# Optimization experiments

Measured on AMD Instinct MI355X. Metric: run time of the kernel, lower is better.

Reference implementation:

```python
import jax, jax.numpy as jnp
import numpy as np

B, N, E = 256, 10000, 160000
H1, H2 = 1024, 128


def setup_inputs() -> dict:
    key = jax.random.key(0)
    ks = jax.random.split(key, 8)
    data = jax.random.normal(ks[0], (B, N), dtype=jnp.float32)
    edge_index = jax.random.randint(ks[1], (2, E), 0, N, dtype=jnp.int64)
    # GCNConv(1, 1): scalar weight + scalar bias (Glorot-ish init)
    gcn_w = jax.random.normal(ks[2], (1,), dtype=jnp.float32)
    gcn_b = jnp.zeros((1,), dtype=jnp.float32)
    # encoder: Linear(N, 1024) -> ReLU -> Linear(1024, 128) -> ReLU
    W1 = jax.random.normal(ks[3], (N, H1), dtype=jnp.float32) * (1.0 / np.sqrt(N))
    b1 = jnp.zeros((H1,), dtype=jnp.float32)
    W2 = jax.random.normal(ks[4], (H1, H2), dtype=jnp.float32) * (1.0 / np.sqrt(H1))
    b2 = jnp.zeros((H2,), dtype=jnp.float32)
    return {"data": data, "gcn_w": gcn_w, "gcn_b": gcn_b,
            "W1": W1, "b1": b1, "W2": W2, "b2": b2,
            "edge_index": edge_index}


def reference(data, gcn_w, gcn_b, W1, b1, W2, b2, edge_index):
    n = data.shape[1]
    # PyG GCNConv defaults: add self-loops, symmetric normalization.
    loop = jnp.arange(n, dtype=edge_index.dtype)
    src = jnp.concatenate([edge_index[0], loop])  # [E+N]
    dst = jnp.concatenate([edge_index[1], loop])
    deg = jax.ops.segment_sum(jnp.ones_like(dst, dtype=data.dtype), dst,
                              num_segments=n)  # >= 1 thanks to self-loops
    dinv = jax.lax.rsqrt(deg)
    norm = dinv[src] * dinv[dst]  # [E+N]
    # linear on 1-dim node features == scalar multiply, batched over B samples
    xw = data * gcn_w[0]                      # [B, N]
    msgs = xw[:, src] * norm                  # [B, E+N]
    agg = jax.ops.segment_sum(msgs.T, dst, num_segments=n).T  # [B, N]
    g = jax.nn.relu(agg + gcn_b[0])           # relu'd GCN output, one row per sample
    # dense MLP encoder (p_drop = 0 so dropout is identity)
    h = jax.nn.relu(g @ W1 + b1)              # [B, 1024]
    return jax.nn.relu(h @ W2 + b2)           # [B, 128]
```

## Files before the change

kernel.cpp:

```cpp
#include <hip/hip_runtime.h>
#include <hip/hip_bf16.h>


#define KPAD 10240
#define NSTEPS 10
#define ZSPLIT 16
#define ELLW 64

typedef __attribute__((ext_vector_type(8))) short short8v;
typedef __attribute__((ext_vector_type(4))) float f32x4;

__device__ inline short f2bf(float f) {
    union { float f; unsigned u; } v; v.f = f;
    unsigned r = v.u + 0x7fffu + ((v.u >> 16) & 1u);
    return (short)(r >> 16);
}

__device__ inline float bf2f(short s) {
    union { unsigned u; float f; } v;
    v.u = ((unsigned)(unsigned short)s) << 16;
    return v.f;
}

__device__ inline void gll16(const short* g, short* l) {
    __builtin_amdgcn_global_load_lds(
        (const __attribute__((address_space(1))) void*)g,
        (__attribute__((address_space(3))) void*)l, 16, 0, 0);
}

__global__ void pack_kernel(const float* __restrict__ data, const float* __restrict__ gw,
                            short* __restrict__ xwT, const float* __restrict__ W1,
                            short* __restrict__ W1T, float4* __restrict__ cntz,
                            int N, int B, int H1, int tTiles, int cTiles) {
    __shared__ short tile[32][66];
    int id = blockIdx.x, t = threadIdx.x;
    if (id < tTiles) {
        int nt = (N + 31) >> 5;
        int xb = id % nt, yb = id / nt;
        int n0 = xb * 32, b0 = yb * 32;
        float w = gw[0];
        int tx = t & 31, ty = t >> 5;
#pragma unroll
        for (int i = 0; i < 4; ++i) {
            int b = b0 + ty + i * 8;
            int n = n0 + tx;
            float v = (n < N) ? data[(size_t)b * N + n] : 0.f;
            tile[ty + i * 8][tx] = f2bf(v * w);
        }
        __syncthreads();
#pragma unroll
        for (int i = 0; i < 4; ++i) {
            int n = n0 + ty + i * 8;
            if (n < N) xwT[(size_t)n * B + b0 + tx] = tile[tx][ty + i * 8];
        }
    } else if (id < tTiles + cTiles) {
        int c = id - tTiles;
        int nk = KPAD >> 6;
        int kx = c % nk, hy = c / nk;
        int k0 = kx * 64, h0 = hy * 32;
        int hl = t & 31, kr = t >> 5;
#pragma unroll
        for (int i = 0; i < 8; ++i) {
            int k = k0 + kr + i * 8;
            float v = (k < N) ? W1[(size_t)k * H1 + h0 + hl] : 0.f;
            tile[hl][kr + i * 8] = f2bf(v);
        }
        __syncthreads();
        int kl = t & 63, hr = t >> 6;
#pragma unroll
        for (int i = 0; i < 8; ++i) {
            int h = h0 + hr + i * 4;
            W1T[(size_t)h * KPAD + k0 + kl] = tile[hr + i * 4][kl];
        }
    } else {
        int i = (id - tTiles - cTiles) * 256 + t;
        cntz[i] = make_float4(0.f, 0.f, 0.f, 0.f);
    }
}

__global__ void ell_fill(const int* __restrict__ ei, int* __restrict__ cnt,
                         int* __restrict__ ell, int E) {
    int e = blockIdx.x * blockDim.x + threadIdx.x;
    if (e >= E) return;
    int s = ei[e], d = ei[E + e];
    int c = atomicAdd(&cnt[d], 1);
    if (c < ELLW) ell[(d << 6) + c] = s;
}

__global__ void gather_kernel(const int* __restrict__ cnt, const int* __restrict__ ell,
                              const float* __restrict__ gcn_b, const short* __restrict__ xwT,
                              short* __restrict__ A0, int N, int B) {
    int row = blockIdx.x * 4 + (threadIdx.x >> 6);
    if (row >= N) return;
    int lane = threadIdx.x & 63;
    const short4* x4 = (const short4*)xwT;
    const int B4 = B >> 2;
    float gb = gcn_b[0];
    int dcnt = cnt[row];
    float di = rsqrtf((float)dcnt + 1.0f);
    float w = di * di;
    short4 v = x4[(size_t)row * B4 + lane];
    float ax = bf2f(v.x) * w, ay = bf2f(v.y) * w, az = bf2f(v.z) * w, aw = bf2f(v.w) * w;
    const int* er = ell + ((size_t)row << 6);
    int m = dcnt < ELLW ? dcnt : ELLW;
    int i = 0;
    for (; i + 1 < m; i += 2) {
        int s0 = er[i], s1 = er[i + 1];
        float n0 = rsqrtf((float)cnt[s0] + 1.0f) * di;
        float n1 = rsqrtf((float)cnt[s1] + 1.0f) * di;
        short4 u0 = x4[(size_t)s0 * B4 + lane];
        short4 u1 = x4[(size_t)s1 * B4 + lane];
        ax = fmaf(bf2f(u0.x), n0, ax); ay = fmaf(bf2f(u0.y), n0, ay);
        az = fmaf(bf2f(u0.z), n0, az); aw = fmaf(bf2f(u0.w), n0, aw);
        ax = fmaf(bf2f(u1.x), n1, ax); ay = fmaf(bf2f(u1.y), n1, ay);
        az = fmaf(bf2f(u1.z), n1, az); aw = fmaf(bf2f(u1.w), n1, aw);
    }
    if (i < m) {
        int s0 = er[i];
        float n0 = rsqrtf((float)cnt[s0] + 1.0f) * di;
        short4 u0 = x4[(size_t)s0 * B4 + lane];
        ax = fmaf(bf2f(u0.x), n0, ax); ay = fmaf(bf2f(u0.y), n0, ay);
        az = fmaf(bf2f(u0.z), n0, az); aw = fmaf(bf2f(u0.w), n0, aw);
    }
    short4 s4;
    s4.x = f2bf(fmaxf(ax + gb, 0.f));
    s4.y = f2bf(fmaxf(ay + gb, 0.f));
    s4.z = f2bf(fmaxf(az + gb, 0.f));
    s4.w = f2bf(fmaxf(aw + gb, 0.f));
    ((short4*)(A0 + (size_t)row * B))[lane] = s4;
}

__global__ void convertA(const short* __restrict__ A0, short* __restrict__ A, int K, int M) {
    __shared__ short tile[32][34];
    int k0 = blockIdx.x * 32, m0 = blockIdx.y * 32;
    int tx = threadIdx.x, ty = threadIdx.y;
#pragma unroll
    for (int i = 0; i < 4; ++i) {
        int k = k0 + ty + i * 8;
        short v = (k < K) ? A0[(size_t)k * M + m0 + tx] : (short)0;
        tile[tx][ty + i * 8] = v;
    }
    __syncthreads();
#pragma unroll
    for (int i = 0; i < 4; ++i) {
        int m = m0 + ty + i * 8;
        A[(size_t)m * KPAD + k0 + tx] = tile[ty + i * 8][tx];
    }
}

__global__ void __launch_bounds__(512)
gemm1_mfma(const short* __restrict__ A, const short* __restrict__ Wt,
           float* __restrict__ hpart) {
    __shared__ __align__(16) short ldsA[2][8192];
    __shared__ __align__(16) short ldsB[2][8192];
    const int n0 = blockIdx.x * 128;
    const int m0 = blockIdx.y * 128;
    const int kz = blockIdx.z * (NSTEPS * 64);
    const int t = threadIdx.x;
    const int l = t & 63, w = t >> 6;
    const int wm = w >> 2, wn = w & 3;
    const int q = l >> 4, i16 = l & 15;

    const int sRow = t & 127, sKq = t >> 7;
    const short* gA = A + (size_t)(m0 + sRow) * KPAD + kz + sKq * 8;
    const short* gB = Wt + (size_t)(n0 + sRow) * KPAD + kz + sKq * 8;
    const int ld0 = w * 512;
    const int ld1 = 4096 + w * 512;

    f32x4 acc[4][2];
#pragma unroll
    for (int mi = 0; mi < 4; ++mi)
#pragma unroll
        for (int ni = 0; ni < 2; ++ni) acc[mi][ni] = (f32x4){0.f, 0.f, 0.f, 0.f};

    gll16(gA, &ldsA[0][ld0]); gll16(gA + 32, &ldsA[0][ld1]);
    gll16(gB, &ldsB[0][ld0]); gll16(gB + 32, &ldsB[0][ld1]);
    gA += 64; gB += 64;

    for (int ks = 0; ks < NSTEPS; ++ks) {
        const int cur = ks & 1;
        if (ks + 1 < NSTEPS) {
            gll16(gA, &ldsA[cur ^ 1][ld0]); gll16(gA + 32, &ldsA[cur ^ 1][ld1]);
            gll16(gB, &ldsB[cur ^ 1][ld0]); gll16(gB + 32, &ldsB[cur ^ 1][ld1]);
            gA += 64; gB += 64;
            asm volatile("s_waitcnt vmcnt(4)" ::: "memory");
        } else {
            asm volatile("s_waitcnt vmcnt(0)" ::: "memory");
        }
        __builtin_amdgcn_s_barrier();
        __builtin_amdgcn_sched_barrier(0);
        const short* bA = &ldsA[cur][0];
        const short* bB = &ldsB[cur][0];
#pragma unroll
        for (int kh = 0; kh < 2; ++kh) {
            const int kq = kh * 4 + q;
            short8v a[4], b[2];
#pragma unroll
            for (int mi = 0; mi < 4; ++mi)
                a[mi] = *(const short8v*)&bA[kq * 1024 + (wm * 64 + mi * 16 + i16) * 8];
#pragma unroll
            for (int ni = 0; ni < 2; ++ni)
                b[ni] = *(const short8v*)&bB[kq * 1024 + (wn * 32 + ni * 16 + i16) * 8];
#pragma unroll
            for (int mi = 0; mi < 4; ++mi)
#pragma unroll
                for (int ni = 0; ni < 2; ++ni)
                    acc[mi][ni] = __builtin_amdgcn_mfma_f32_16x16x32_bf16(a[mi], b[ni], acc[mi][ni], 0, 0, 0);
        }
        __builtin_amdgcn_s_barrier();
    }

    float* hp = hpart + (size_t)blockIdx.z * (256 * 1024);
#pragma unroll
    for (int mi = 0; mi < 4; ++mi) {
#pragma unroll
        for (int ni = 0; ni < 2; ++ni) {
#pragma unroll
            for (int r = 0; r < 4; ++r) {
                int mr = m0 + wm * 64 + mi * 16 + q * 4 + r;
                int nc = n0 + wn * 32 + ni * 16 + i16;
                hp[(size_t)mr * 1024 + nc] = acc[mi][ni][r];
            }
        }
    }
}

__global__ void gemm2_fused(const float* __restrict__ hpart, const float* __restrict__ b1,
                            const float* __restrict__ W2, const float* __restrict__ b2,
                            float* __restrict__ out, int Z) {
    __shared__ float h_lds[1024];
    __shared__ float partial[8][128];
    int b = blockIdx.x, t = threadIdx.x;
    float s = 0.f;
    for (int z = 0; z < Z; ++z) s += hpart[(size_t)z * (256 * 1024) + b * 1024 + t];
    h_lds[t] = fmaxf(s + b1[t], 0.f);
    __syncthreads();
    int j = t & 127, oct = t >> 7;
    const float* w2p = W2 + (size_t)oct * 128 * 128 + j;
    const float* hp = h_lds + oct * 128;
    float s0 = 0.f, s1 = 0.f, s2 = 0.f, s3 = 0.f;
#pragma unroll 8
    for (int k = 0; k < 128; k += 4) {
        s0 = fmaf(hp[k],     w2p[(size_t)k * 128],       s0);
        s1 = fmaf(hp[k + 1], w2p[(size_t)(k + 1) * 128], s1);
        s2 = fmaf(hp[k + 2], w2p[(size_t)(k + 2) * 128], s2);
        s3 = fmaf(hp[k + 3], w2p[(size_t)(k + 3) * 128], s3);
    }
    partial[oct][j] = (s0 + s1) + (s2 + s3);
    __syncthreads();
    if (t < 128) {
        float v = b2[t];
#pragma unroll
        for (int o = 0; o < 8; ++o) v += partial[o][t];
        out[(size_t)b * 128 + t] = fmaxf(v, 0.f);
    }
}

extern "C" void kernel_launch(void* const* d_in, const int* in_sizes, int n_in,
                              void* d_out, int out_size, void* d_ws, size_t ws_size,
                              hipStream_t stream) {
    const float* data = (const float*)d_in[0];
    const float* gw   = (const float*)d_in[1];
    const float* gb   = (const float*)d_in[2];
    const float* W1   = (const float*)d_in[3];
    const float* b1   = (const float*)d_in[4];
    const float* W2   = (const float*)d_in[5];
    const float* b2   = (const float*)d_in[6];
    const int*   ei   = (const int*)d_in[7];
    float* out = (float*)d_out;

    const int B  = 256;
    const int H1 = in_sizes[4];
    const int H2 = in_sizes[6];
    const int N  = in_sizes[3] / H1;
    const int E  = in_sizes[7] / 2;
    const int NP = 10240;

    int* iws = (int*)d_ws;
    int*   cnt  = iws;
    int*   ell  = cnt + NP;
    short* S    = (short*)(ell + (size_t)NP * ELLW);
    short* A    = S;
    short* W1T  = A + (size_t)256 * KPAD;
    short* xwT  = W1T + (size_t)1024 * KPAD;
    short* A0   = xwT + (size_t)N * B;
    float* hpart = (float*)xwT;

    const int tTiles = ((N + 31) / 32) * (B / 32);
    const int cTiles = (KPAD / 64) * (H1 / 32);
    const int zBlks  = NP / 1024;

    pack_kernel<<<tTiles + cTiles + zBlks, 256, 0, stream>>>(
        data, gw, xwT, W1, W1T, (float4*)cnt, N, B, H1, tTiles, cTiles);

    ell_fill<<<(E + 255) / 256, 256, 0, stream>>>(ei, cnt, ell, E);

    gather_kernel<<<(N + 3) / 4, 256, 0, stream>>>(cnt, ell, gb, xwT, A0, N, B);

    convertA<<<dim3(KPAD / 32, B / 32), dim3(32, 8), 0, stream>>>(A0, A, N, B);

    dim3 g1(H1 / 128, B / 128, ZSPLIT);
    gemm1_mfma<<<g1, 512, 0, stream>>>(A, W1T, hpart);

    gemm2_fused<<<B, 1024, 0, stream>>>(hpart, b1, W2, b2, out, ZSPLIT);
}
```

Measured before the change: 88.00 us.

## Fuse all stages into one persistent kernel with software grid barriers

```diff
diff --git a/kernel.cpp b/kernel.cpp
--- a/kernel.cpp
+++ b/kernel.cpp
@@ -6,253 +6,303 @@
 #define NSTEPS 10
 #define ZSPLIT 16
 #define ELLW 64
+#define NP 10240
+#define NBLK 256
+#define NTHR 512
 
 typedef __attribute__((ext_vector_type(8))) short short8v;
 typedef __attribute__((ext_vector_type(4))) float f32x4;
 
-__device__ inline short f2bf(float f) {
+__device__ __forceinline__ short f2bf(float f) {
     union { float f; unsigned u; } v; v.f = f;
     unsigned r = v.u + 0x7fffu + ((v.u >> 16) & 1u);
     return (short)(r >> 16);
 }
 
-__device__ inline float bf2f(short s) {
+__device__ __forceinline__ float bf2f(short s) {
     union { unsigned u; float f; } v;
     v.u = ((unsigned)(unsigned short)s) << 16;
     return v.f;
 }
 
-__device__ inline void gll16(const short* g, short* l) {
+__device__ __forceinline__ void gll16(const short* g, short* l) {
     __builtin_amdgcn_global_load_lds(
         (const __attribute__((address_space(1))) void*)g,
         (__attribute__((address_space(3))) void*)l, 16, 0, 0);
 }
 
-__global__ void pack_kernel(const float* __restrict__ data, const float* __restrict__ gw,
-                            short* __restrict__ xwT, const float* __restrict__ W1,
-                            short* __restrict__ W1T, float4* __restrict__ cntz,
-                            int N, int B, int H1, int tTiles, int cTiles) {
-    __shared__ short tile[32][66];
-    int id = blockIdx.x, t = threadIdx.x;
-    if (id < tTiles) {
-        int nt = (N + 31) >> 5;
-        int xb = id % nt, yb = id / nt;
-        int n0 = xb * 32, b0 = yb * 32;
-        float w = gw[0];
-        int tx = t & 31, ty = t >> 5;
-#pragma unroll
-        for (int i = 0; i < 4; ++i) {
-            int b = b0 + ty + i * 8;
-            int n = n0 + tx;
-            float v = (n < N) ? data[(size_t)b * N + n] : 0.f;
-            tile[ty + i * 8][tx] = f2bf(v * w);
-        }
-        __syncthreads();
-#pragma unroll
-        for (int i = 0; i < 4; ++i) {
-            int n = n0 + ty + i * 8;
-            if (n < N) xwT[(size_t)n * B + b0 + tx] = tile[tx][ty + i * 8];
-        }
-    } else if (id < tTiles + cTiles) {
-        int c = id - tTiles;
-        int nk = KPAD >> 6;
-        int kx = c % nk, hy = c / nk;
-        int k0 = kx * 64, h0 = hy * 32;
-        int hl = t & 31, kr = t >> 5;
-#pragma unroll
-        for (int i = 0; i < 8; ++i) {
-            int k = k0 + kr + i * 8;
-            float v = (k < N) ? W1[(size_t)k * H1 + h0 + hl] : 0.f;
-            tile[hl][kr + i * 8] = f2bf(v);
-        }
-        __syncthreads();
-        int kl = t & 63, hr = t >> 6;
-#pragma unroll
-        for (int i = 0; i < 8; ++i) {
-            int h = h0 + hr + i * 4;
-            W1T[(size_t)h * KPAD + k0 + kl] = tile[hr + i * 4][kl];
-        }
-    } else {
-        int i = (id - tTiles - cTiles) * 256 + t;
-        cntz[i] = make_float4(0.f, 0.f, 0.f, 0.f);
-    }
-}
-
-__global__ void ell_fill(const int* __restrict__ ei, int* __restrict__ cnt,
-                         int* __restrict__ ell, int E) {
-    int e = blockIdx.x * blockDim.x + threadIdx.x;
-    if (e >= E) return;
-    int s = ei[e], d = ei[E + e];
-    int c = atomicAdd(&cnt[d], 1);
-    if (c < ELLW) ell[(d << 6) + c] = s;
-}
-
-__global__ void gather_kernel(const int* __restrict__ cnt, const int* __restrict__ ell,
-                              const float* __restrict__ gcn_b, const short* __restrict__ xwT,
-                              short* __restrict__ A0, int N, int B) {
-    int row = blockIdx.x * 4 + (threadIdx.x >> 6);
-    if (row >= N) return;
-    int lane = threadIdx.x & 63;
-    const short4* x4 = (const short4*)xwT;
-    const int B4 = B >> 2;
-    float gb = gcn_b[0];
-    int dcnt = cnt[row];
-    float di = rsqrtf((float)dcnt + 1.0f);
-    float w = di * di;
-    short4 v = x4[(size_t)row * B4 + lane];
-    float ax = bf2f(v.x) * w, ay = bf2f(v.y) * w, az = bf2f(v.z) * w, aw = bf2f(v.w) * w;
-    const int* er = ell + ((size_t)row << 6);
-    int m = dcnt < ELLW ? dcnt : ELLW;
-    int i = 0;
-    for (; i + 1 < m; i += 2) {
-        int s0 = er[i], s1 = er[i + 1];
-        float n0 = rsqrtf((float)cnt[s0] + 1.0f) * di;
-        float n1 = rsqrtf((float)cnt[s1] + 1.0f) * di;
-        short4 u0 = x4[(size_t)s0 * B4 + lane];
-        short4 u1 = x4[(size_t)s1 * B4 + lane];
-        ax = fmaf(bf2f(u0.x), n0, ax); ay = fmaf(bf2f(u0.y), n0, ay);
-        az = fmaf(bf2f(u0.z), n0, az); aw = fmaf(bf2f(u0.w), n0, aw);
-        ax = fmaf(bf2f(u1.x), n1, ax); ay = fmaf(bf2f(u1.y), n1, ay);
-        az = fmaf(bf2f(u1.z), n1, az); aw = fmaf(bf2f(u1.w), n1, aw);
-    }
-    if (i < m) {
-        int s0 = er[i];
-        float n0 = rsqrtf((float)cnt[s0] + 1.0f) * di;
-        short4 u0 = x4[(size_t)s0 * B4 + lane];
-        ax = fmaf(bf2f(u0.x), n0, ax); ay = fmaf(bf2f(u0.y), n0, ay);
-        az = fmaf(bf2f(u0.z), n0, az); aw = fmaf(bf2f(u0.w), n0, aw);
-    }
-    short4 s4;
-    s4.x = f2bf(fmaxf(ax + gb, 0.f));
-    s4.y = f2bf(fmaxf(ay + gb, 0.f));
-    s4.z = f2bf(fmaxf(az + gb, 0.f));
-    s4.w = f2bf(fmaxf(aw + gb, 0.f));
-    ((short4*)(A0 + (size_t)row * B))[lane] = s4;
-}
-
-__global__ void convertA(const short* __restrict__ A0, short* __restrict__ A, int K, int M) {
-    __shared__ short tile[32][34];
-    int k0 = blockIdx.x * 32, m0 = blockIdx.y * 32;
-    int tx = threadIdx.x, ty = threadIdx.y;
-#pragma unroll
-    for (int i = 0; i < 4; ++i) {
-        int k = k0 + ty + i * 8;
-        short v = (k < K) ? A0[(size_t)k * M + m0 + tx] : (short)0;
-        tile[tx][ty + i * 8] = v;
-    }
+__global__ void init_bar(int* bar) {
+    if (threadIdx.x < 2) bar[threadIdx.x] = 0;
+}
+
+__device__ __forceinline__ void gridbar(int* bar) {
     __syncthreads();
-#pragma unroll
-    for (int i = 0; i < 4; ++i) {
-        int m = m0 + ty + i * 8;
-        A[(size_t)m * KPAD + k0 + tx] = tile[ty + i * 8][tx];
-    }
-}
-
-__global__ void __launch_bounds__(512)
-gemm1_mfma(const short* __restrict__ A, const short* __restrict__ Wt,
-           float* __restrict__ hpart) {
+    if (threadIdx.x == 0) {
+        __threadfence();
+        int gen = __hip_atomic_load(&bar[1], __ATOMIC_RELAXED, __HIP_MEMORY_SCOPE_AGENT);
+        int old = atomicAdd(&bar[0], 1);
+        if (old == NBLK - 1) {
+            atomicExch(&bar[0], 0);
+            __threadfence();
+            atomicAdd(&bar[1], 1);
+        } else {
+            while (__hip_atomic_load(&bar[1], __ATOMIC_ACQUIRE,
+                                     __HIP_MEMORY_SCOPE_AGENT) == gen)
+                __builtin_amdgcn_s_sleep(4);
+        }
+        __threadfence();
+    }
+    __syncthreads();
+}
+
+__global__ void __launch_bounds__(NTHR, 1)
+mega(const float* __restrict__ data, const float* __restrict__ gw,
+     const float* __restrict__ gb, const float* __restrict__ W1,
+     const float* __restrict__ b1, const float* __restrict__ W2,
+     const float* __restrict__ b2, const int* __restrict__ ei,
+     float* __restrict__ out,
+     int* cnt, int* ell, int* bar,
+     short* A, short* W1T, short* xwT, short* A0, float* hpart,
+     int N, int B, int H1, int E) {
     __shared__ __align__(16) short ldsA[2][8192];
     __shared__ __align__(16) short ldsB[2][8192];
-    const int n0 = blockIdx.x * 128;
-    const int m0 = blockIdx.y * 128;
-    const int kz = blockIdx.z * (NSTEPS * 64);
     const int t = threadIdx.x;
-    const int l = t & 63, w = t >> 6;
-    const int wm = w >> 2, wn = w & 3;
-    const int q = l >> 4, i16 = l & 15;
-
-    const int sRow = t & 127, sKq = t >> 7;
-    const short* gA = A + (size_t)(m0 + sRow) * KPAD + kz + sKq * 8;
-    const short* gB = Wt + (size_t)(n0 + sRow) * KPAD + kz + sKq * 8;
-    const int ld0 = w * 512;
-    const int ld1 = 4096 + w * 512;
-
-    f32x4 acc[4][2];
-#pragma unroll
-    for (int mi = 0; mi < 4; ++mi)
-#pragma unroll
-        for (int ni = 0; ni < 2; ++ni) acc[mi][ni] = (f32x4){0.f, 0.f, 0.f, 0.f};
-
-    gll16(gA, &ldsA[0][ld0]); gll16(gA + 32, &ldsA[0][ld1]);
-    gll16(gB, &ldsB[0][ld0]); gll16(gB + 32, &ldsB[0][ld1]);
-    gA += 64; gB += 64;
-
-    for (int ks = 0; ks < NSTEPS; ++ks) {
-        const int cur = ks & 1;
-        if (ks + 1 < NSTEPS) {
-            gll16(gA, &ldsA[cur ^ 1][ld0]); gll16(gA + 32, &ldsA[cur ^ 1][ld1]);
-            gll16(gB, &ldsB[cur ^ 1][ld0]); gll16(gB + 32, &ldsB[cur ^ 1][ld1]);
-            gA += 64; gB += 64;
-            asm volatile("s_waitcnt vmcnt(4)" ::: "memory");
-        } else {
-            asm volatile("s_waitcnt vmcnt(0)" ::: "memory");
-        }
-        __builtin_amdgcn_s_barrier();
-        __builtin_amdgcn_sched_barrier(0);
-        const short* bA = &ldsA[cur][0];
-        const short* bB = &ldsB[cur][0];
-#pragma unroll
-        for (int kh = 0; kh < 2; ++kh) {
-            const int kq = kh * 4 + q;
-            short8v a[4], b[2];
-#pragma unroll
-            for (int mi = 0; mi < 4; ++mi)
-                a[mi] = *(const short8v*)&bA[kq * 1024 + (wm * 64 + mi * 16 + i16) * 8];
+    const int blk = blockIdx.x;
+
+    {
+        short (*tl34)[34] = (short(*)[34])&ldsA[0][0];
+        short (*tl66)[66] = (short(*)[66])&ldsB[0][0];
+        const int nt = (N + 31) >> 5;
+        const int tTiles = nt * (B >> 5);
+        const int cTiles = (KPAD >> 6) * (H1 >> 5);
+        const int zTiles = (NP / 4) / NTHR;
+        const int total = tTiles + cTiles + zTiles;
+        const float w = gw[0];
+        for (int id = blk; id < total; id += NBLK) {
+            if (id < tTiles) {
+                int xb = id % nt, yb = id / nt;
+                int n0 = xb * 32, b0 = yb * 32;
+                int tx = t & 31, ty = t >> 5;
+#pragma unroll
+                for (int i = 0; i < 2; ++i) {
+                    int b = b0 + ty + i * 16;
+                    int n = n0 + tx;
+                    float v = (n < N) ? data[(size_t)b * N + n] : 0.f;
+                    tl34[ty + i * 16][tx] = f2bf(v * w);
+                }
+                __syncthreads();
+#pragma unroll
+                for (int i = 0; i < 2; ++i) {
+                    int n = n0 + ty + i * 16;
+                    if (n < N) xwT[(size_t)n * B + b0 + tx] = tl34[tx][ty + i * 16];
+                }
+                __syncthreads();
+            } else if (id < tTiles + cTiles) {
+                int c = id - tTiles;
+                int nk = KPAD >> 6;
+                int kx = c % nk, hy = c / nk;
+                int k0 = kx * 64, h0 = hy * 32;
+                int hl = t & 31, kr = t >> 5;
+#pragma unroll
+                for (int i = 0; i < 4; ++i) {
+                    int k = k0 + kr + i * 16;
+                    float v = (k < N) ? W1[(size_t)k * H1 + h0 + hl] : 0.f;
+                    tl66[hl][kr + i * 16] = f2bf(v);
+                }
+                __syncthreads();
+                int kl = t & 63, hr = t >> 6;
+#pragma unroll
+                for (int i = 0; i < 4; ++i) {
+                    int h = h0 + hr + i * 8;
+                    W1T[(size_t)h * KPAD + k0 + kl] = tl66[hr + i * 8][kl];
+                }
+                __syncthreads();
+            } else {
+                int i = (id - tTiles - cTiles) * NTHR + t;
+                ((float4*)cnt)[i] = make_float4(0.f, 0.f, 0.f, 0.f);
+            }
+        }
+    }
+    gridbar(bar);
+
+    for (int e = blk * NTHR + t; e < E; e += NBLK * NTHR) {
+        int s = ei[e], d = ei[E + e];
+        int c = atomicAdd(&cnt[d], 1);
+        if (c < ELLW) ell[(d << 6) + c] = s;
+    }
+    gridbar(bar);
+
+    {
+        const int lane = t & 63;
+        const short4* x4 = (const short4*)xwT;
+        const int B4 = B >> 2;
+        const float gbv = gb[0];
+        for (int row = blk * 8 + (t >> 6); row < N; row += NBLK * 8) {
+            int dcnt = cnt[row];
+            float di = rsqrtf((float)dcnt + 1.0f);
+            float w = di * di;
+            short4 v = x4[(size_t)row * B4 + lane];
+            float ax = bf2f(v.x) * w, ay = bf2f(v.y) * w;
+            float az = bf2f(v.z) * w, aw = bf2f(v.w) * w;
+            const int* er = ell + ((size_t)row << 6);
+            int m = dcnt < ELLW ? dcnt : ELLW;
+            int i = 0;
+            for (; i + 1 < m; i += 2) {
+                int s0 = er[i], s1 = er[i + 1];
+                float n0 = rsqrtf((float)cnt[s0] + 1.0f) * di;
+                float n1 = rsqrtf((float)cnt[s1] + 1.0f) * di;
+                short4 u0 = x4[(size_t)s0 * B4 + lane];
+                short4 u1 = x4[(size_t)s1 * B4 + lane];
+                ax = fmaf(bf2f(u0.x), n0, ax); ay = fmaf(bf2f(u0.y), n0, ay);
+                az = fmaf(bf2f(u0.z), n0, az); aw = fmaf(bf2f(u0.w), n0, aw);
+                ax = fmaf(bf2f(u1.x), n1, ax); ay = fmaf(bf2f(u1.y), n1, ay);
+                az = fmaf(bf2f(u1.z), n1, az); aw = fmaf(bf2f(u1.w), n1, aw);
+            }
+            if (i < m) {
+                int s0 = er[i];
+                float n0 = rsqrtf((float)cnt[s0] + 1.0f) * di;
+                short4 u0 = x4[(size_t)s0 * B4 + lane];
+                ax = fmaf(bf2f(u0.x), n0, ax); ay = fmaf(bf2f(u0.y), n0, ay);
+                az = fmaf(bf2f(u0.z), n0, az); aw = fmaf(bf2f(u0.w), n0, aw);
+            }
+            short4 s4;
+            s4.x = f2bf(fmaxf(ax + gbv, 0.f));
+            s4.y = f2bf(fmaxf(ay + gbv, 0.f));
+            s4.z = f2bf(fmaxf(az + gbv, 0.f));
+            s4.w = f2bf(fmaxf(aw + gbv, 0.f));
+            ((short4*)(A0 + (size_t)row * B))[lane] = s4;
+        }
+    }
+    gridbar(bar);
+
+    {
+        short (*tl34)[34] = (short(*)[34])&ldsA[0][0];
+        const int nkx = KPAD >> 5;
+        const int tiles = nkx * (B >> 5);
+        const int tx = t & 31, ty = t >> 5;
+        for (int id = blk; id < tiles; id += NBLK) {
+            int kx = id % nkx, my = id / nkx;
+            int k0 = kx * 32, m0 = my * 32;
+#pragma unroll
+            for (int i = 0; i < 2; ++i) {
+                int k = k0 + ty + i * 16;
+                short v = (k < N) ? A0[(size_t)k * B + m0 + tx] : (short)0;
+                tl34[tx][ty + i * 16] = v;
+            }
+            __syncthreads();
+#pragma unroll
+            for (int i = 0; i < 2; ++i) {
+                int m = m0 + ty + i * 16;
+                A[(size_t)m * KPAD + k0 + tx] = tl34[ty + i * 16][tx];
+            }
+            __syncthreads();
+        }
+    }
+    gridbar(bar);
+
+    {
+        const int n0 = (blk & 7) * 128;
+        const int m0 = ((blk >> 3) & 1) * 128;
+        const int kz = (blk >> 4) * (NSTEPS * 64);
+        const int l = t & 63, w = t >> 6;
+        const int wm = w >> 2, wn = w & 3;
+        const int q = l >> 4, i16 = l & 15;
+
+        const int sRow = t & 127, sKq = t >> 7;
+        const short* gA = A + (size_t)(m0 + sRow) * KPAD + kz + sKq * 8;
+        const short* gB = W1T + (size_t)(n0 + sRow) * KPAD + kz + sKq * 8;
+        const int ld0 = w * 512;
+        const int ld1 = 4096 + w * 512;
+
+        f32x4 acc[4][2];
+#pragma unroll
+        for (int mi = 0; mi < 4; ++mi)
+#pragma unroll
+            for (int ni = 0; ni < 2; ++ni) acc[mi][ni] = (f32x4){0.f, 0.f, 0.f, 0.f};
+
+        gll16(gA, &ldsA[0][ld0]); gll16(gA + 32, &ldsA[0][ld1]);
+        gll16(gB, &ldsB[0][ld0]); gll16(gB + 32, &ldsB[0][ld1]);
+        gA += 64; gB += 64;
+
+        for (int ks = 0; ks < NSTEPS; ++ks) {
+            const int cur = ks & 1;
+            if (ks + 1 < NSTEPS) {
+                gll16(gA, &ldsA[cur ^ 1][ld0]); gll16(gA + 32, &ldsA[cur ^ 1][ld1]);
+                gll16(gB, &ldsB[cur ^ 1][ld0]); gll16(gB + 32, &ldsB[cur ^ 1][ld1]);
+                gA += 64; gB += 64;
+                asm volatile("s_waitcnt vmcnt(4)" ::: "memory");
+            } else {
+                asm volatile("s_waitcnt vmcnt(0)" ::: "memory");
+            }
+            __builtin_amdgcn_s_barrier();
+            __builtin_amdgcn_sched_barrier(0);
+            const short* bA = &ldsA[cur][0];
+            const short* bB = &ldsB[cur][0];
+#pragma unroll
+            for (int kh = 0; kh < 2; ++kh) {
+                const int kq = kh * 4 + q;
+                short8v a[4], b[2];
+#pragma unroll
+                for (int mi = 0; mi < 4; ++mi)
+                    a[mi] = *(const short8v*)&bA[kq * 1024 + (wm * 64 + mi * 16 + i16) * 8];
+#pragma unroll
+                for (int ni = 0; ni < 2; ++ni)
+                    b[ni] = *(const short8v*)&bB[kq * 1024 + (wn * 32 + ni * 16 + i16) * 8];
+#pragma unroll
+                for (int mi = 0; mi < 4; ++mi)
+#pragma unroll
+                    for (int ni = 0; ni < 2; ++ni)
+                        acc[mi][ni] = __builtin_amdgcn_mfma_f32_16x16x32_bf16(a[mi], b[ni], acc[mi][ni], 0, 0, 0);
+            }
+            __builtin_amdgcn_s_barrier();
+        }
+
+        float* hp = hpart + (size_t)(blk >> 4) * (256 * 1024);
+#pragma unroll
+        for (int mi = 0; mi < 4; ++mi)
 #pragma unroll
             for (int ni = 0; ni < 2; ++ni)
-                b[ni] = *(const short8v*)&bB[kq * 1024 + (wn * 32 + ni * 16 + i16) * 8];
-#pragma unroll
-            for (int mi = 0; mi < 4; ++mi)
-#pragma unroll
-                for (int ni = 0; ni < 2; ++ni)
-                    acc[mi][ni] = __builtin_amdgcn_mfma_f32_16x16x32_bf16(a[mi], b[ni], acc[mi][ni], 0, 0, 0);
-        }
-        __builtin_amdgcn_s_barrier();
-    }
-
-    float* hp = hpart + (size_t)blockIdx.z * (256 * 1024);
-#pragma unroll
-    for (int mi = 0; mi < 4; ++mi) {
-#pragma unroll
-        for (int ni = 0; ni < 2; ++ni) {
-#pragma unroll
-            for (int r = 0; r < 4; ++r) {
-                int mr = m0 + wm * 64 + mi * 16 + q * 4 + r;
-                int nc = n0 + wn * 32 + ni * 16 + i16;
-                hp[(size_t)mr * 1024 + nc] = acc[mi][ni][r];
-            }
-        }
-    }
-}
-
-__global__ void gemm2_fused(const float* __restrict__ hpart, const float* __restrict__ b1,
-                            const float* __restrict__ W2, const float* __restrict__ b2,
-                            float* __restrict__ out, int Z) {
-    __shared__ float h_lds[1024];
-    __shared__ float partial[8][128];
-    int b = blockIdx.x, t = threadIdx.x;
-    float s = 0.f;
-    for (int z = 0; z < Z; ++z) s += hpart[(size_t)z * (256 * 1024) + b * 1024 + t];
-    h_lds[t] = fmaxf(s + b1[t], 0.f);
-    __syncthreads();
-    int j = t & 127, oct = t >> 7;
-    const float* w2p = W2 + (size_t)oct * 128 * 128 + j;
-    const float* hp = h_lds + oct * 128;
-    float s0 = 0.f, s1 = 0.f, s2 = 0.f, s3 = 0.f;
+#pragma unroll
+                for (int r = 0; r < 4; ++r) {
+                    int mr = m0 + wm * 64 + mi * 16 + q * 4 + r;
+                    int nc = n0 + wn * 32 + ni * 16 + i16;
+                    hp[(size_t)mr * 1024 + nc] = acc[mi][ni][r];
+                }
+    }
+    gridbar(bar);
+
+    {
+        float* h_lds = (float*)&ldsA[0][0];
+        float (*partial)[128] = (float(*)[128])&ldsB[0][0];
+        const int b = blk;
+#pragma unroll
+        for (int i = 0; i < 2; ++i) {
+            int col = t + i * NTHR;
+            float s = 0.f;
+            for (int z = 0; z < ZSPLIT; ++z)
+                s += hpart[(size_t)z * (256 * 1024) + (size_t)b * 1024 + col];
+            h_lds[col] = fmaxf(s + b1[col], 0.f);
+        }
+        __syncthreads();
+        int j = t & 127, oct = t >> 7;
+        const float* w2p = W2 + (size_t)(oct * 256) * 128 + j;
+        const float* hp = h_lds + oct * 256;
+        float s0 = 0.f, s1 = 0.f, s2 = 0.f, s3 = 0.f;
 #pragma unroll 8
-    for (int k = 0; k < 128; k += 4) {
-        s0 = fmaf(hp[k],     w2p[(size_t)k * 128],       s0);
-        s1 = fmaf(hp[k + 1], w2p[(size_t)(k + 1) * 128], s1);
-        s2 = fmaf(hp[k + 2], w2p[(size_t)(k + 2) * 128], s2);
-        s3 = fmaf(hp[k + 3], w2p[(size_t)(k + 3) * 128], s3);
-    }
-    partial[oct][j] = (s0 + s1) + (s2 + s3);
-    __syncthreads();
-    if (t < 128) {
-        float v = b2[t];
-#pragma unroll
-        for (int o = 0; o < 8; ++o) v += partial[o][t];
-        out[(size_t)b * 128 + t] = fmaxf(v, 0.f);
+        for (int k = 0; k < 256; k += 4) {
+            s0 = fmaf(hp[k],     w2p[(size_t)k * 128],       s0);
+            s1 = fmaf(hp[k + 1], w2p[(size_t)(k + 1) * 128], s1);
+            s2 = fmaf(hp[k + 2], w2p[(size_t)(k + 2) * 128], s2);
+            s3 = fmaf(hp[k + 3], w2p[(size_t)(k + 3) * 128], s3);
+        }
+        partial[oct][j] = (s0 + s1) + (s2 + s3);
+        __syncthreads();
+        if (t < 128) {
+            float v = b2[t];
+#pragma unroll
+            for (int o = 0; o < 4; ++o) v += partial[o][t];
+            out[(size_t)b * 128 + t] = fmaxf(v, 0.f);
+        }
     }
 }
 
@@ -274,33 +324,21 @@
     const int H2 = in_sizes[6];
     const int N  = in_sizes[3] / H1;
     const int E  = in_sizes[7] / 2;
-    const int NP = 10240;
+    (void)H2;
 
     int* iws = (int*)d_ws;
     int*   cnt  = iws;
     int*   ell  = cnt + NP;
-    short* S    = (short*)(ell + (size_t)NP * ELLW);
+    int*   bar  = ell + (size_t)NP * ELLW;
+    short* S    = (short*)(bar + 4);
     short* A    = S;
     short* W1T  = A + (size_t)256 * KPAD;
     short* xwT  = W1T + (size_t)1024 * KPAD;
     short* A0   = xwT + (size_t)N * B;
     float* hpart = (float*)xwT;
 
-    const int tTiles = ((N + 31) / 32) * (B / 32);
-    const int cTiles = (KPAD / 64) * (H1 / 32);
-    const int zBlks  = NP / 1024;
-
-    pack_kernel<<<tTiles + cTiles + zBlks, 256, 0, stream>>>(
-        data, gw, xwT, W1, W1T, (float4*)cnt, N, B, H1, tTiles, cTiles);
-
-    ell_fill<<<(E + 255) / 256, 256, 0, stream>>>(ei, cnt, ell, E);
-
-    gather_kernel<<<(N + 3) / 4, 256, 0, stream>>>(cnt, ell, gb, xwT, A0, N, B);
-
-    convertA<<<dim3(KPAD / 32, B / 32), dim3(32, 8), 0, stream>>>(A0, A, N, B);
-
-    dim3 g1(H1 / 128, B / 128, ZSPLIT);
-    gemm1_mfma<<<g1, 512, 0, stream>>>(A, W1T, hpart);
-
-    gemm2_fused<<<B, 1024, 0, stream>>>(hpart, b1, W2, b2, out, ZSPLIT);
-}
+    init_bar<<<1, 64, 0, stream>>>(bar);
+    mega<<<NBLK, NTHR, 0, stream>>>(data, gw, gb, W1, b1, W2, b2, ei, out,
+                                    cnt, ell, bar, A, W1T, xwT, A0, hpart,
+                                    N, B, H1, E);
+}
```

New measurement: 325.9 us. 270% more time.

## Fuse GEMM1 and GEMM2 into one kernel with a software grid barrier

Applied to the files above, without the earlier changes.

```diff
diff --git a/kernel.cpp b/kernel.cpp
--- a/kernel.cpp
+++ b/kernel.cpp
@@ -6,6 +6,7 @@
 #define NSTEPS 10
 #define ZSPLIT 16
 #define ELLW 64
+#define NP 10240
 
 typedef __attribute__((ext_vector_type(8))) short short8v;
 typedef __attribute__((ext_vector_type(4))) float f32x4;
@@ -31,6 +32,7 @@
 __global__ void pack_kernel(const float* __restrict__ data, const float* __restrict__ gw,
                             short* __restrict__ xwT, const float* __restrict__ W1,
                             short* __restrict__ W1T, float4* __restrict__ cntz,
+                            int* __restrict__ bar,
                             int N, int B, int H1, int tTiles, int cTiles) {
     __shared__ short tile[32][66];
     int id = blockIdx.x, t = threadIdx.x;
@@ -73,8 +75,10 @@
             W1T[(size_t)h * KPAD + k0 + kl] = tile[hr + i * 4][kl];
         }
     } else {
-        int i = (id - tTiles - cTiles) * 256 + t;
+        int zb = id - tTiles - cTiles;
+        int i = zb * 256 + t;
         cntz[i] = make_float4(0.f, 0.f, 0.f, 0.f);
+        if (zb == 0 && t < 8) bar[t] = 0;
     }
 }
 
@@ -148,111 +152,137 @@
     }
 }
 
+__device__ inline void gridbar256(int* bar) {
+    __syncthreads();
+    if (threadIdx.x == 0) {
+        __threadfence();
+        int gen = __hip_atomic_load(&bar[0], __ATOMIC_RELAXED, __HIP_MEMORY_SCOPE_AGENT);
+        int old = atomicAdd(&bar[1], 1);
+        if (old == 255) {
+            bar[1] = 0;
+            __threadfence();
+            atomicAdd(&bar[0], 1);
+        } else {
+            while (__hip_atomic_load(&bar[0], __ATOMIC_ACQUIRE,
+                                     __HIP_MEMORY_SCOPE_AGENT) == gen)
+                __builtin_amdgcn_s_sleep(2);
+        }
+        __threadfence();
+    }
+    __syncthreads();
+}
+
 __global__ void __launch_bounds__(512)
-gemm1_mfma(const short* __restrict__ A, const short* __restrict__ Wt,
-           float* __restrict__ hpart) {
+gemm12_kernel(const short* __restrict__ A, const short* __restrict__ Wt,
+              float* __restrict__ hpart, const float* __restrict__ b1,
+              const float* __restrict__ W2, const float* __restrict__ b2,
+              float* __restrict__ out, int* __restrict__ bar) {
     __shared__ __align__(16) short ldsA[2][8192];
     __shared__ __align__(16) short ldsB[2][8192];
-    const int n0 = blockIdx.x * 128;
-    const int m0 = blockIdx.y * 128;
-    const int kz = blockIdx.z * (NSTEPS * 64);
     const int t = threadIdx.x;
-    const int l = t & 63, w = t >> 6;
-    const int wm = w >> 2, wn = w & 3;
-    const int q = l >> 4, i16 = l & 15;
-
-    const int sRow = t & 127, sKq = t >> 7;
-    const short* gA = A + (size_t)(m0 + sRow) * KPAD + kz + sKq * 8;
-    const short* gB = Wt + (size_t)(n0 + sRow) * KPAD + kz + sKq * 8;
-    const int ld0 = w * 512;
-    const int ld1 = 4096 + w * 512;
-
-    f32x4 acc[4][2];
-#pragma unroll
-    for (int mi = 0; mi < 4; ++mi)
-#pragma unroll
-        for (int ni = 0; ni < 2; ++ni) acc[mi][ni] = (f32x4){0.f, 0.f, 0.f, 0.f};
-
-    gll16(gA, &ldsA[0][ld0]); gll16(gA + 32, &ldsA[0][ld1]);
-    gll16(gB, &ldsB[0][ld0]); gll16(gB + 32, &ldsB[0][ld1]);
-    gA += 64; gB += 64;
-
-    for (int ks = 0; ks < NSTEPS; ++ks) {
-        const int cur = ks & 1;
-        if (ks + 1 < NSTEPS) {
-            gll16(gA, &ldsA[cur ^ 1][ld0]); gll16(gA + 32, &ldsA[cur ^ 1][ld1]);
-            gll16(gB, &ldsB[cur ^ 1][ld0]); gll16(gB + 32, &ldsB[cur ^ 1][ld1]);
-            gA += 64; gB += 64;
-            asm volatile("s_waitcnt vmcnt(4)" ::: "memory");
-        } else {
-            asm volatile("s_waitcnt vmcnt(0)" ::: "memory");
-        }
-        __builtin_amdgcn_s_barrier();
-        __builtin_amdgcn_sched_barrier(0);
-        const short* bA = &ldsA[cur][0];
-        const short* bB = &ldsB[cur][0];
-#pragma unroll
-        for (int kh = 0; kh < 2; ++kh) {
-            const int kq = kh * 4 + q;
-            short8v a[4], b[2];
-#pragma unroll
-            for (int mi = 0; mi < 4; ++mi)
-                a[mi] = *(const short8v*)&bA[kq * 1024 + (wm * 64 + mi * 16 + i16) * 8];
+    const int blk = blockIdx.x;
+    {
+        const int n0 = (blk & 7) * 128;
+        const int m0 = ((blk >> 3) & 1) * 128;
+        const int kz = (blk >> 4) * (NSTEPS * 64);
+        const int l = t & 63, w = t >> 6;
+        const int wm = w >> 2, wn = w & 3;
+        const int q = l >> 4, i16 = l & 15;
+
+        const int sRow = t & 127, sKq = t >> 7;
+        const short* gA = A + (size_t)(m0 + sRow) * KPAD + kz + sKq * 8;
+        const short* gB = Wt + (size_t)(n0 + sRow) * KPAD + kz + sKq * 8;
+        const int ld0 = w * 512;
+        const int ld1 = 4096 + w * 512;
+
+        f32x4 acc[4][2];
+#pragma unroll
+        for (int mi = 0; mi < 4; ++mi)
+#pragma unroll
+            for (int ni = 0; ni < 2; ++ni) acc[mi][ni] = (f32x4){0.f, 0.f, 0.f, 0.f};
+
+        gll16(gA, &ldsA[0][ld0]); gll16(gA + 32, &ldsA[0][ld1]);
+        gll16(gB, &ldsB[0][ld0]); gll16(gB + 32, &ldsB[0][ld1]);
+        gA += 64; gB += 64;
+
+        for (int ks = 0; ks < NSTEPS; ++ks) {
+            const int cur = ks & 1;
+            if (ks + 1 < NSTEPS) {
+                gll16(gA, &ldsA[cur ^ 1][ld0]); gll16(gA + 32, &ldsA[cur ^ 1][ld1]);
+                gll16(gB, &ldsB[cur ^ 1][ld0]); gll16(gB + 32, &ldsB[cur ^ 1][ld1]);
+                gA += 64; gB += 64;
+                asm volatile("s_waitcnt vmcnt(4)" ::: "memory");
+            } else {
+                asm volatile("s_waitcnt vmcnt(0)" ::: "memory");
+            }
+            __builtin_amdgcn_s_barrier();
+            __builtin_amdgcn_sched_barrier(0);
+            const short* bA = &ldsA[cur][0];
+            const short* bB = &ldsB[cur][0];
+#pragma unroll
+            for (int kh = 0; kh < 2; ++kh) {
+                const int kq = kh * 4 + q;
+                short8v a[4], b[2];
+#pragma unroll
+                for (int mi = 0; mi < 4; ++mi)
+                    a[mi] = *(const short8v*)&bA[kq * 1024 + (wm * 64 + mi * 16 + i16) * 8];
+#pragma unroll
+                for (int ni = 0; ni < 2; ++ni)
+                    b[ni] = *(const short8v*)&bB[kq * 1024 + (wn * 32 + ni * 16 + i16) * 8];
+#pragma unroll
+                for (int mi = 0; mi < 4; ++mi)
+#pragma unroll
+                    for (int ni = 0; ni < 2; ++ni)
+                        acc[mi][ni] = __builtin_amdgcn_mfma_f32_16x16x32_bf16(a[mi], b[ni], acc[mi][ni], 0, 0, 0);
+            }
+            __builtin_amdgcn_s_barrier();
+        }
+
+        float* hp = hpart + (size_t)(blk >> 4) * (256 * 1024);
+#pragma unroll
+        for (int mi = 0; mi < 4; ++mi)
 #pragma unroll
             for (int ni = 0; ni < 2; ++ni)
-                b[ni] = *(const short8v*)&bB[kq * 1024 + (wn * 32 + ni * 16 + i16) * 8];
-#pragma unroll
-            for (int mi = 0; mi < 4; ++mi)
-#pragma unroll
-                for (int ni = 0; ni < 2; ++ni)
-                    acc[mi][ni] = __builtin_amdgcn_mfma_f32_16x16x32_bf16(a[mi], b[ni], acc[mi][ni], 0, 0, 0);
-        }
-        __builtin_amdgcn_s_barrier();
-    }
-
-    float* hp = hpart + (size_t)blockIdx.z * (256 * 1024);
-#pragma unroll
-    for (int mi = 0; mi < 4; ++mi) {
-#pragma unroll
-        for (int ni = 0; ni < 2; ++ni) {
-#pragma unroll
-            for (int r = 0; r < 4; ++r) {
-                int mr = m0 + wm * 64 + mi * 16 + q * 4 + r;
-                int nc = n0 + wn * 32 + ni * 16 + i16;
-                hp[(size_t)mr * 1024 + nc] = acc[mi][ni][r];
-            }
-        }
-    }
-}
-
-__global__ void gemm2_fused(const float* __restrict__ hpart, const float* __restrict__ b1,
-                            const float* __restrict__ W2, const float* __restrict__ b2,
-                            float* __restrict__ out, int Z) {
-    __shared__ float h_lds[1024];
-    __shared__ float partial[8][128];
-    int b = blockIdx.x, t = threadIdx.x;
-    float s = 0.f;
-    for (int z = 0; z < Z; ++z) s += hpart[(size_t)z * (256 * 1024) + b * 1024 + t];
-    h_lds[t] = fmaxf(s + b1[t], 0.f);
-    __syncthreads();
-    int j = t & 127, oct = t >> 7;
-    const float* w2p = W2 + (size_t)oct * 128 * 128 + j;
-    const float* hp = h_lds + oct * 128;
-    float s0 = 0.f, s1 = 0.f, s2 = 0.f, s3 = 0.f;
+#pragma unroll
+                for (int r = 0; r < 4; ++r) {
+                    int mr = m0 + wm * 64 + mi * 16 + q * 4 + r;
+                    int nc = n0 + wn * 32 + ni * 16 + i16;
+                    hp[(size_t)mr * 1024 + nc] = acc[mi][ni][r];
+                }
+    }
+    gridbar256(bar);
+    {
+        float* h_lds = (float*)&ldsA[0][0];
+        float (*partial)[128] = (float(*)[128])&ldsB[0][0];
+        const int b = blk;
+#pragma unroll
+        for (int i = 0; i < 2; ++i) {
+            int col = t + i * 512;
+            float s = 0.f;
+            for (int z = 0; z < ZSPLIT; ++z)
+                s += hpart[(size_t)z * (256 * 1024) + (size_t)b * 1024 + col];
+            h_lds[col] = fmaxf(s + b1[col], 0.f);
+        }
+        __syncthreads();
+        int j = t & 127, oct = t >> 7;
+        const float* w2p = W2 + (size_t)(oct * 256) * 128 + j;
+        const float* hp = h_lds + oct * 256;
+        float s0 = 0.f, s1 = 0.f, s2 = 0.f, s3 = 0.f;
 #pragma unroll 8
-    for (int k = 0; k < 128; k += 4) {
-        s0 = fmaf(hp[k],     w2p[(size_t)k * 128],       s0);
-        s1 = fmaf(hp[k + 1], w2p[(size_t)(k + 1) * 128], s1);
-        s2 = fmaf(hp[k + 2], w2p[(size_t)(k + 2) * 128], s2);
-        s3 = fmaf(hp[k + 3], w2p[(size_t)(k + 3) * 128], s3);
-    }
-    partial[oct][j] = (s0 + s1) + (s2 + s3);
-    __syncthreads();
-    if (t < 128) {
-        float v = b2[t];
-#pragma unroll
-        for (int o = 0; o < 8; ++o) v += partial[o][t];
-        out[(size_t)b * 128 + t] = fmaxf(v, 0.f);
+        for (int k = 0; k < 256; k += 4) {
+            s0 = fmaf(hp[k],     w2p[(size_t)k * 128],       s0);
+            s1 = fmaf(hp[k + 1], w2p[(size_t)(k + 1) * 128], s1);
+            s2 = fmaf(hp[k + 2], w2p[(size_t)(k + 2) * 128], s2);
+            s3 = fmaf(hp[k + 3], w2p[(size_t)(k + 3) * 128], s3);
+        }
+        partial[oct][j] = (s0 + s1) + (s2 + s3);
+        __syncthreads();
+        if (t < 128) {
+            float v = b2[t];
+#pragma unroll
+            for (int o = 0; o < 4; ++o) v += partial[o][t];
+            out[(size_t)b * 128 + t] = fmaxf(v, 0.f);
+        }
     }
 }
 
@@ -274,12 +304,13 @@
     const int H2 = in_sizes[6];
     const int N  = in_sizes[3] / H1;
     const int E  = in_sizes[7] / 2;
-    const int NP = 10240;
+    (void)H2;
 
     int* iws = (int*)d_ws;
     int*   cnt  = iws;
     int*   ell  = cnt + NP;
-    short* S    = (short*)(ell + (size_t)NP * ELLW);
+    int*   bar  = ell + (size_t)NP * ELLW;
+    short* S    = (short*)(bar + 8);
     short* A    = S;
     short* W1T  = A + (size_t)256 * KPAD;
     short* xwT  = W1T + (size_t)1024 * KPAD;
@@ -291,7 +322,7 @@
     const int zBlks  = NP / 1024;
 
     pack_kernel<<<tTiles + cTiles + zBlks, 256, 0, stream>>>(
-        data, gw, xwT, W1, W1T, (float4*)cnt, N, B, H1, tTiles, cTiles);
+        data, gw, xwT, W1, W1T, (float4*)cnt, bar, N, B, H1, tTiles, cTiles);
 
     ell_fill<<<(E + 255) / 256, 256, 0, stream>>>(ei, cnt, ell, E);
 
@@ -299,8 +330,5 @@
 
     convertA<<<dim3(KPAD / 32, B / 32), dim3(32, 8), 0, stream>>>(A0, A, N, B);
 
-    dim3 g1(H1 / 128, B / 128, ZSPLIT);
-    gemm1_mfma<<<g1, 512, 0, stream>>>(A, W1T, hpart);
-
-    gemm2_fused<<<B, 1024, 0, stream>>>(hpart, b1, W2, b2, out, ZSPLIT);
-}
+    gemm12_kernel<<<256, 512, 0, stream>>>(A, W1T, hpart, b1, W2, b2, out, bar);
+}
```

After: 135.8 us. 54.3% more time.
